# Optimization experiments

Hardware: AMD Instinct MI355X
Metric: run time of the kernel (lower is better)

## Reference

```python
import jax, jax.numpy as jnp
import numpy as np

EPS = 1e-3  # Keras LayerNormalization default epsilon


def _gru_seq(x_tbf, W, U, b):
    """Keras GRU (reset_after=True). x_tbf: [T,B,F], W: [F,3U], U: [U,3U], b: [2,3U]."""
    bi, br = b[0], b[1]
    xw = jnp.einsum('tbf,fg->tbg', x_tbf, W) + bi  # precompute input projections
    B = x_tbf.shape[1]
    units = U.shape[0]
    h0 = jnp.zeros((B, units), x_tbf.dtype)

    def step(h, xw_t):
        inner = h @ U + br
        xz, xr, xh = jnp.split(xw_t, 3, axis=-1)
        rz, rr, rh = jnp.split(inner, 3, axis=-1)
        z = jax.nn.sigmoid(xz + rz)
        r = jax.nn.sigmoid(xr + rr)
        hh = jnp.tanh(xh + r * rh)
        h_new = z * h + (1.0 - z) * hh
        return h_new, h_new

    _, hs = jax.lax.scan(step, h0, xw)
    return hs  # [T,B,U]


def setup_inputs() -> dict:
    key = jax.random.key(0)
    B, T, F, Uu = 64, 1024, 256, 512
    ks = jax.random.split(key, 8)
    s = 0.05
    return {
        'x': jax.random.normal(ks[0], (B, T, F), jnp.float32),
        'Wf': jax.random.normal(ks[1], (F, 3 * Uu), jnp.float32) * s,
        'Uf': jax.random.normal(ks[2], (Uu, 3 * Uu), jnp.float32) * s,
        'bf': jnp.zeros((2, 3 * Uu), jnp.float32),
        'Wb': jax.random.normal(ks[3], (F, 3 * Uu), jnp.float32) * s,
        'Ub': jax.random.normal(ks[4], (Uu, 3 * Uu), jnp.float32) * s,
        'bb': jnp.zeros((2, 3 * Uu), jnp.float32),
        'Wp': jax.random.normal(ks[5], (F, 2 * Uu), jnp.float32) * s,
        'gamma': jnp.ones((2 * Uu,), jnp.float32),
        'beta': jnp.zeros((2 * Uu,), jnp.float32),
    }


def reference(x, Wf, Uf, bf, Wb, Ub, bb, Wp, gamma, beta):
    x_t = jnp.transpose(x, (1, 0, 2))  # [T,B,F]
    hf = _gru_seq(x_t, Wf, Uf, bf)
    hb = _gru_seq(x_t[::-1], Wb, Ub, bb)[::-1]
    gru_out = jnp.transpose(jnp.concatenate([hf, hb], axis=-1), (1, 0, 2))  # [B,T,2U]
    residual = x @ Wp  # projection (F != 2U)
    y = gru_out + residual
    mu = jnp.mean(y, axis=-1, keepdims=True)
    var = jnp.var(y, axis=-1, keepdims=True)
    return gamma * (y - mu) * jax.lax.rsqrt(var + EPS) + beta
```

## Files before the change

kernel.cpp:

```cpp
#include <hip/hip_runtime.h>
#include <stdint.h>
#include <stddef.h>

#define TB 1024
#define NBATCH 64
#define FD 256
#define UD 512
#define G3 1536
#define OD 1024

#define WS_BAR 0
#define WS_H 512
#define WS_RESID (512 + 4 * NBATCH * UD * 2)

#define NREC 64
#define NRESID 16384

typedef __bf16 v8bf __attribute__((ext_vector_type(8)));
typedef float v4f __attribute__((ext_vector_type(4)));

__device__ __forceinline__ v4f mfma16(v8bf a, v8bf b, v4f c) {
  return __builtin_amdgcn_mfma_f32_16x16x32_bf16(a, b, c, 0, 0, 0);
}

__device__ __forceinline__ float sigf(float x) {
  return 1.0f / (1.0f + __expf(-x));
}
__device__ __forceinline__ float tanhf_fast(float x) {
  float ax = fabsf(x);
  float e = __expf(-2.0f * ax);
  float t = (1.0f - e) / (1.0f + e);
  return copysignf(t, x);
}

__device__ __forceinline__ v8bf cvt8(const float* p) {
  float4 a = *(const float4*)p;
  float4 b = *(const float4*)(p + 4);
  v8bf r;
  r[0] = (__bf16)a.x; r[1] = (__bf16)a.y; r[2] = (__bf16)a.z; r[3] = (__bf16)a.w;
  r[4] = (__bf16)b.x; r[5] = (__bf16)b.y; r[6] = (__bf16)b.z; r[7] = (__bf16)b.w;
  return r;
}

struct XW { v4f a0, a1, a2; };

__device__ __forceinline__ XW compute_xw(const float* __restrict__ x,
                                         const v8bf wfr[8][3],
                                         float bi0, float bi1, float bi2,
                                         int b, int t, int quad) {
  XW r;
  r.a0 = v4f{bi0, bi0, bi0, bi0};
  r.a1 = v4f{bi1, bi1, bi1, bi1};
  r.a2 = v4f{bi2, bi2, bi2, bi2};
  const float* xp = x + ((size_t)b * TB + t) * FD + quad * 8;
#pragma unroll
  for (int ki = 0; ki < 8; ++ki) {
    v8bf xa = cvt8(xp + ki * 32);
    r.a0 = mfma16(xa, wfr[ki][0], r.a0);
    r.a1 = mfma16(xa, wfr[ki][1], r.a1);
    r.a2 = mfma16(xa, wfr[ki][2], r.a2);
  }
  return r;
}

__device__ void recurrent_body(const float* __restrict__ x,
                               const float* __restrict__ Wd,
                               const float* __restrict__ Ud,
                               const float* __restrict__ bd,
                               float* __restrict__ out,
                               char* __restrict__ ws, int bx) {
  const int dir = bx >> 5;
  const int j0 = (bx & 31) * 16;
  const int tid = threadIdx.x;
  const int lane = tid & 63;
  const int col16 = lane & 15;
  const int quad = lane >> 4;
  const int m0 = (tid >> 6) * 16;

  uint32_t* bar = (uint32_t*)(ws + WS_BAR);
  __bf16* h0 = (__bf16*)(ws + WS_H) + (size_t)dir * 2 * NBATCH * UD;
  __bf16* h1 = h0 + NBATCH * UD;

  v8bf ufr[16][3];
#pragma unroll
  for (int ki = 0; ki < 16; ++ki) {
#pragma unroll
    for (int g = 0; g < 3; ++g) {
      const float* p = Ud + (size_t)(ki * 32 + quad * 8) * G3 + g * UD + j0 + col16;
      v8bf v;
#pragma unroll
      for (int e = 0; e < 8; ++e) v[e] = (__bf16)p[(size_t)e * G3];
      ufr[ki][g] = v;
    }
  }
  v8bf wfr[8][3];
#pragma unroll
  for (int ki = 0; ki < 8; ++ki) {
#pragma unroll
    for (int g = 0; g < 3; ++g) {
      const float* p = Wd + (size_t)(ki * 32 + quad * 8) * G3 + g * UD + j0 + col16;
      v8bf v;
#pragma unroll
      for (int e = 0; e < 8; ++e) v[e] = (__bf16)p[(size_t)e * G3];
      wfr[ki][g] = v;
    }
  }
  const float bi0 = bd[0 * UD + j0 + col16];
  const float bi1 = bd[1 * UD + j0 + col16];
  const float bi2 = bd[2 * UD + j0 + col16];
  const float br0 = bd[G3 + 0 * UD + j0 + col16];
  const float br1 = bd[G3 + 1 * UD + j0 + col16];
  const float br2 = bd[G3 + 2 * UD + j0 + col16];

  const int tstep = dir ? -1 : 1;
  int t = dir ? (TB - 1) : 0;
  XW cur = compute_xw(x, wfr, bi0, bi1, bi2, m0 + col16, t, quad);

  int p = 0;
  for (int s = 0; s < TB; ++s) {
    const __bf16* hcur = (p == 0) ? h0 : h1;
    __bf16* hnxt = (p == 0) ? h1 : h0;

    v4f au0 = v4f{br0, br0, br0, br0};
    v4f au1 = v4f{br1, br1, br1, br1};
    v4f au2 = v4f{br2, br2, br2, br2};
    if (s > 0) {
      const __bf16* hrow = hcur + (size_t)(m0 + col16) * UD + quad * 8;
#pragma unroll
      for (int ki = 0; ki < 16; ++ki) {
        v8bf ha = *(const v8bf*)(hrow + ki * 32);
        au0 = mfma16(ha, ufr[ki][0], au0);
        au1 = mfma16(ha, ufr[ki][1], au1);
        au2 = mfma16(ha, ufr[ki][2], au2);
      }
    }

    float hn[4];
#pragma unroll
    for (int r = 0; r < 4; ++r) {
      const int brow = m0 + quad * 4 + r;
      float hold = (s > 0) ? (float)hcur[(size_t)brow * UD + j0 + col16] : 0.0f;
      float z = sigf(cur.a0[r] + au0[r]);
      float rg = sigf(cur.a1[r] + au1[r]);
      float hh = tanhf_fast(cur.a2[r] + rg * au2[r]);
      float v = z * hold + (1.0f - z) * hh;
      hn[r] = v;
      __builtin_nontemporal_store(
          v, out + ((size_t)brow * TB + t) * OD + dir * UD + j0 + col16);
    }

    if (s < TB - 1) {
#pragma unroll
      for (int r = 0; r < 4; ++r) {
        const int brow = m0 + quad * 4 + r;
        hnxt[(size_t)brow * UD + j0 + col16] = (__bf16)hn[r];
      }
      __syncthreads();
      if (tid == 0) {
        __hip_atomic_fetch_add(bar, 1u, __ATOMIC_RELEASE, __HIP_MEMORY_SCOPE_AGENT);
      }
      t += tstep;
      XW nxt = compute_xw(x, wfr, bi0, bi1, bi2, m0 + col16, t, quad);
      if (tid == 0) {
        const uint32_t target = (uint32_t)NREC * (uint32_t)(s + 1);
        while (__hip_atomic_load(bar, __ATOMIC_ACQUIRE, __HIP_MEMORY_SCOPE_AGENT) < target) {
        }
      }
      __syncthreads();
      cur = nxt;
      p ^= 1;
    }
  }
}

__device__ void resid_body(const float* __restrict__ x,
                           const float* __restrict__ Wp,
                           __bf16* __restrict__ resid, int rb) {
  const int mb = rb & 1023;
  const int nb = rb >> 10;
  const int tid = threadIdx.x;
  const int lane = tid & 63;
  const int col16 = lane & 15;
  const int quad = lane >> 4;
  const int wave = tid >> 6;
  const int wm = wave & 1;
  const int wn = wave >> 1;
  const int rowbase = mb * 64 + wm * 32;
  const int colbase = nb * 64 + wn * 32;

  v4f acc[2][2];
#pragma unroll
  for (int i = 0; i < 2; ++i)
#pragma unroll
    for (int j = 0; j < 2; ++j) acc[i][j] = v4f{0.f, 0.f, 0.f, 0.f};

#pragma unroll
  for (int ki = 0; ki < 8; ++ki) {
    v8bf a0 = cvt8(x + (size_t)(rowbase + col16) * FD + ki * 32 + quad * 8);
    v8bf a1 = cvt8(x + (size_t)(rowbase + 16 + col16) * FD + ki * 32 + quad * 8);
    v8bf b0, b1;
#pragma unroll
    for (int e = 0; e < 8; ++e) {
      const float* wp = Wp + (size_t)(ki * 32 + quad * 8 + e) * OD + colbase + col16;
      b0[e] = (__bf16)wp[0];
      b1[e] = (__bf16)wp[16];
    }
    acc[0][0] = mfma16(a0, b0, acc[0][0]);
    acc[0][1] = mfma16(a0, b1, acc[0][1]);
    acc[1][0] = mfma16(a1, b0, acc[1][0]);
    acc[1][1] = mfma16(a1, b1, acc[1][1]);
  }
#pragma unroll
  for (int mt = 0; mt < 2; ++mt)
#pragma unroll
    for (int nt = 0; nt < 2; ++nt)
#pragma unroll
      for (int r = 0; r < 4; ++r) {
        __builtin_nontemporal_store(
            (__bf16)acc[mt][nt][r],
            resid + (size_t)(rowbase + mt * 16 + quad * 4 + r) * OD + colbase +
                nt * 16 + col16);
      }
}

__global__ __launch_bounds__(256, 1) void mega_kernel(
    const float* __restrict__ x, const float* __restrict__ Wf,
    const float* __restrict__ Uf, const float* __restrict__ bf_,
    const float* __restrict__ Wb, const float* __restrict__ Ub,
    const float* __restrict__ bb_, const float* __restrict__ Wp,
    float* __restrict__ out, char* __restrict__ ws) {
  const int bx = blockIdx.x;
  if (bx < NREC) {
    const int dir = bx >> 5;
    recurrent_body(x, dir ? Wb : Wf, dir ? Ub : Uf, dir ? bb_ : bf_, out, ws, bx);
  } else {
    resid_body(x, Wp, (__bf16*)(ws + WS_RESID), bx - NREC);
  }
}

__global__ __launch_bounds__(256) void ln_kernel(
    const __bf16* __restrict__ resid, const float* __restrict__ gamma,
    const float* __restrict__ beta, float* __restrict__ out) {
  const int row = blockIdx.x * 4 + (threadIdx.x >> 6);
  const int lane = threadIdx.x & 63;
  const float* orow = out + (size_t)row * OD;
  const __bf16* rrow = resid + (size_t)row * OD;

  float y[16];
  float s = 0.f, s2 = 0.f;
#pragma unroll
  for (int i = 0; i < 16; ++i) {
    const int c = lane + 64 * i;
    float v = orow[c] + (float)rrow[c];
    y[i] = v;
    s += v;
    s2 += v * v;
  }
#pragma unroll
  for (int m = 32; m >= 1; m >>= 1) {
    s += __shfl_xor(s, m);
    s2 += __shfl_xor(s2, m);
  }
  const float mu = s * (1.0f / OD);
  const float var = s2 * (1.0f / OD) - mu * mu;
  const float rstd = rsqrtf(var + 1e-3f);
  float* wrow = out + (size_t)row * OD;
#pragma unroll
  for (int i = 0; i < 16; ++i) {
    const int c = lane + 64 * i;
    __builtin_nontemporal_store(gamma[c] * (y[i] - mu) * rstd + beta[c], wrow + c);
  }
}

extern "C" void kernel_launch(void* const* d_in, const int* in_sizes, int n_in,
                              void* d_out, int out_size, void* d_ws,
                              size_t ws_size, hipStream_t stream) {
  const float* x = (const float*)d_in[0];
  const float* Wf = (const float*)d_in[1];
  const float* Uf = (const float*)d_in[2];
  const float* bf_ = (const float*)d_in[3];
  const float* Wb = (const float*)d_in[4];
  const float* Ub = (const float*)d_in[5];
  const float* bb_ = (const float*)d_in[6];
  const float* Wp = (const float*)d_in[7];
  const float* gamma = (const float*)d_in[8];
  const float* beta = (const float*)d_in[9];
  float* out = (float*)d_out;
  char* ws = (char*)d_ws;

  hipMemsetAsync(ws, 0, 512, stream);

  mega_kernel<<<dim3(NREC + NRESID), dim3(256), 0, stream>>>(
      x, Wf, Uf, bf_, Wb, Ub, bb_, Wp, out, ws);

  ln_kernel<<<dim3(65536 / 4), dim3(256), 0, stream>>>(
      (const __bf16*)(ws + WS_RESID), gamma, beta, out);
}
```

Measured before the change: 10.30 ms.

## Replace global counter barrier with per-block flags and per-wave polling

Replaces the single atomic counter barrier, shared by both directions, with one flag per block per direction. Every wave polls the 32 flags of its own direction with a ballot and a short sleep, so the trailing __syncthreads and the single-thread spin go away. The previous hidden state is kept in registers instead of being reloaded from global memory. The output stores are moved after the flag publish so they leave the critical path. The aim is to cut barrier latency and contention on the serial recurrence, at the cost of more polling traffic from every wave.

```diff
diff --git a/kernel.cpp b/kernel.cpp
--- a/kernel.cpp
+++ b/kernel.cpp
@@ -70,14 +70,15 @@
                                float* __restrict__ out,
                                char* __restrict__ ws, int bx) {
   const int dir = bx >> 5;
-  const int j0 = (bx & 31) * 16;
+  const int blk = bx & 31;
+  const int j0 = blk * 16;
   const int tid = threadIdx.x;
   const int lane = tid & 63;
   const int col16 = lane & 15;
   const int quad = lane >> 4;
   const int m0 = (tid >> 6) * 16;
 
-  uint32_t* bar = (uint32_t*)(ws + WS_BAR);
+  uint32_t* flags = (uint32_t*)(ws + WS_BAR) + dir * 32;
   __bf16* h0 = (__bf16*)(ws + WS_H) + (size_t)dir * 2 * NBATCH * UD;
   __bf16* h1 = h0 + NBATCH * UD;
 
@@ -116,6 +117,8 @@
   int t = dir ? (TB - 1) : 0;
   XW cur = compute_xw(x, wfr, bi0, bi1, bi2, m0 + col16, t, quad);
 
+  float hold[4] = {0.f, 0.f, 0.f, 0.f};
+
   int p = 0;
   for (int s = 0; s < TB; ++s) {
     const __bf16* hcur = (p == 0) ? h0 : h1;
@@ -138,37 +141,52 @@
     float hn[4];
 #pragma unroll
     for (int r = 0; r < 4; ++r) {
-      const int brow = m0 + quad * 4 + r;
-      float hold = (s > 0) ? (float)hcur[(size_t)brow * UD + j0 + col16] : 0.0f;
       float z = sigf(cur.a0[r] + au0[r]);
       float rg = sigf(cur.a1[r] + au1[r]);
       float hh = tanhf_fast(cur.a2[r] + rg * au2[r]);
-      float v = z * hold + (1.0f - z) * hh;
+      float v = z * hold[r] + (1.0f - z) * hh;
       hn[r] = v;
-      __builtin_nontemporal_store(
-          v, out + ((size_t)brow * TB + t) * OD + dir * UD + j0 + col16);
-    }
+      hold[r] = v;
+    }
+    const int tcur = t;
 
     if (s < TB - 1) {
+#pragma unroll
+      for (int r = 0; r < 4; ++r) {
+        hnxt[(size_t)(m0 + quad * 4 + r) * UD + j0 + col16] = (__bf16)hn[r];
+      }
+      __syncthreads();
+      if (tid == 0) {
+        __hip_atomic_store(&flags[blk], (uint32_t)(s + 1), __ATOMIC_RELEASE,
+                           __HIP_MEMORY_SCOPE_AGENT);
+      }
 #pragma unroll
       for (int r = 0; r < 4; ++r) {
         const int brow = m0 + quad * 4 + r;
-        hnxt[(size_t)brow * UD + j0 + col16] = (__bf16)hn[r];
-      }
-      __syncthreads();
-      if (tid == 0) {
-        __hip_atomic_fetch_add(bar, 1u, __ATOMIC_RELEASE, __HIP_MEMORY_SCOPE_AGENT);
+        __builtin_nontemporal_store(
+            hn[r], out + ((size_t)brow * TB + tcur) * OD + dir * UD + j0 + col16);
       }
       t += tstep;
       XW nxt = compute_xw(x, wfr, bi0, bi1, bi2, m0 + col16, t, quad);
-      if (tid == 0) {
-        const uint32_t target = (uint32_t)NREC * (uint32_t)(s + 1);
-        while (__hip_atomic_load(bar, __ATOMIC_ACQUIRE, __HIP_MEMORY_SCOPE_AGENT) < target) {
-        }
-      }
-      __syncthreads();
+
+      const uint32_t target = (uint32_t)(s + 1);
+      for (;;) {
+        uint32_t f = __hip_atomic_load(&flags[lane & 31], __ATOMIC_RELAXED,
+                                       __HIP_MEMORY_SCOPE_AGENT);
+        if (__ballot(f >= target) == ~0ull) break;
+        __builtin_amdgcn_s_sleep(1);
+      }
+      __builtin_amdgcn_fence(__ATOMIC_ACQUIRE, "agent");
+
       cur = nxt;
       p ^= 1;
+    } else {
+#pragma unroll
+      for (int r = 0; r < 4; ++r) {
+        const int brow = m0 + quad * 4 + r;
+        __builtin_nontemporal_store(
+            hn[r], out + ((size_t)brow * TB + tcur) * OD + dir * UD + j0 + col16);
+      }
     }
   }
 }
```

New measurement: 10.27 ms. No clear change (-0.3%).
